# Kernel tuning notes

Measured on AMD Instinct MI355X. Metric: run time of the kernel, lower is better.

The kernel has to match this reference:

```python
import jax, jax.numpy as jnp
import numpy as np

N_NODES = 100000
N_EDGES = 2000000
D_IN = 4
HID = 64


def setup_inputs() -> dict:
    key = jax.random.key(0)
    ks = jax.random.split(key, 8)
    node_feats = jax.random.normal(ks[0], (N_NODES, D_IN), dtype=jnp.float32)
    pairs = jax.random.randint(ks[1], (N_EDGES, 2), 0, N_NODES, dtype=jnp.int64)
    # Kaiming-ish init scaling
    W1 = jax.random.normal(ks[2], (D_IN, HID), dtype=jnp.float32) / np.sqrt(D_IN)
    b1 = jnp.zeros((HID,), dtype=jnp.float32)
    W2 = jax.random.normal(ks[3], (HID, HID), dtype=jnp.float32) / np.sqrt(HID)
    b2 = jnp.zeros((HID,), dtype=jnp.float32)
    We1 = jax.random.normal(ks[4], (3 * HID, HID), dtype=jnp.float32) / np.sqrt(3 * HID)
    be1 = jnp.zeros((HID,), dtype=jnp.float32)
    We2 = jax.random.normal(ks[5], (HID, 1), dtype=jnp.float32) / np.sqrt(HID)
    be2 = jnp.zeros((1,), dtype=jnp.float32)
    return {"node_feats": node_feats, "pairs": pairs, "W1": W1, "b1": b1,
            "W2": W2, "b2": b2, "We1": We1, "be1": be1, "We2": We2, "be2": be2}


def reference(node_feats, pairs, W1, b1, W2, b2, We1, be1, We2, be2):
    # node MLP: Linear -> ReLU -> Linear -> ReLU
    H = jax.nn.relu(node_feats @ W1 + b1)      # [N, HID]
    H = jax.nn.relu(H @ W2 + b2)               # [N, HID]
    # vectorized gather over all edge pairs (replaces Python loop)
    hu = H[pairs[:, 0]]                        # [E, HID]
    hv = H[pairs[:, 1]]                        # [E, HID]
    E = jnp.concatenate([hu, hv, jnp.abs(hu - hv)], axis=-1)  # [E, 3*HID]
    # edge MLP: Linear -> ReLU -> Linear, squeeze last dim
    scores = (jax.nn.relu(E @ We1 + be1) @ We2 + be2)[:, 0]   # [E]
    return scores
```

## Files before the change

### kernel.cpp

```cpp
#include <hip/hip_runtime.h>

#define N_NODES 100000
#define N_EDGES 2000000

typedef __bf16 bf16x8 __attribute__((ext_vector_type(8)));
typedef float f32x4 __attribute__((ext_vector_type(4)));
typedef float f32x16 __attribute__((ext_vector_type(16)));

__device__ __forceinline__ unsigned f2bf_rne(float f) {
  unsigned u = __builtin_bit_cast(unsigned, f);
  u += 0x7FFFu + ((u >> 16) & 1u);
  return u >> 16;
}

__device__ __forceinline__ unsigned pack_rhu(float lo, float hi) {
  unsigned ulo = __builtin_bit_cast(unsigned, lo) + 0x8000u;
  unsigned uhi = __builtin_bit_cast(unsigned, hi) + 0x8000u;
  return __builtin_amdgcn_perm(uhi, ulo, 0x07060302u);
}

__device__ __forceinline__ unsigned absdiff_pack(unsigned a, unsigned b) {
  float alo = __builtin_bit_cast(float, a << 16);
  float ahi = __builtin_bit_cast(float, a & 0xFFFF0000u);
  float blo = __builtin_bit_cast(float, b << 16);
  float bhi = __builtin_bit_cast(float, b & 0xFFFF0000u);
  return pack_rhu(fabsf(alo - blo), fabsf(ahi - bhi));
}

__global__ __launch_bounds__(64, 1) void node_mfma_kernel(
    const float* __restrict__ X, const float* __restrict__ W1,
    const float* __restrict__ b1, const float* __restrict__ W2,
    const float* __restrict__ b2, unsigned short* __restrict__ H) {
  const int lane = threadIdx.x;
  const int l15 = lane & 15;
  const int quad = lane >> 4;

  float w1v[2][4][8], b1v[2][8];
#pragma unroll
  for (int c = 0; c < 2; ++c)
#pragma unroll
    for (int j = 0; j < 8; ++j) {
      int col = c * 32 + quad * 8 + j;
      b1v[c][j] = b1[col];
#pragma unroll
      for (int d = 0; d < 4; ++d) w1v[c][d][j] = W1[d * 64 + col];
    }

  uint4 afr[2][4];
#pragma unroll
  for (int c = 0; c < 2; ++c)
#pragma unroll
    for (int mt = 0; mt < 4; ++mt) {
      unsigned w[4];
#pragma unroll
      for (int p = 0; p < 4; ++p) {
        int k = c * 32 + quad * 8 + 2 * p;
        unsigned lo = f2bf_rne(W2[k * 64 + mt * 16 + l15]);
        unsigned hi = f2bf_rne(W2[(k + 1) * 64 + mt * 16 + l15]);
        w[p] = lo | (hi << 16);
      }
      afr[c][mt] = make_uint4(w[0], w[1], w[2], w[3]);
    }
  float b2v[16];
#pragma unroll
  for (int mt = 0; mt < 4; ++mt)
#pragma unroll
    for (int r = 0; r < 4; ++r) b2v[mt * 4 + r] = b2[mt * 16 + quad * 4 + r];

  const int ntiles = N_NODES / 16;
  for (int tile = blockIdx.x; tile < ntiles; tile += gridDim.x) {
    float4 xv = ((const float4*)X)[tile * 16 + l15];

    uint4 bfr[2];
#pragma unroll
    for (int c = 0; c < 2; ++c) {
      unsigned w[4];
#pragma unroll
      for (int p = 0; p < 4; ++p) {
        float h0 = fmaxf(b1v[c][2 * p] + xv.x * w1v[c][0][2 * p] +
                             xv.y * w1v[c][1][2 * p] + xv.z * w1v[c][2][2 * p] +
                             xv.w * w1v[c][3][2 * p],
                         0.f);
        float h1 = fmaxf(b1v[c][2 * p + 1] + xv.x * w1v[c][0][2 * p + 1] +
                             xv.y * w1v[c][1][2 * p + 1] +
                             xv.z * w1v[c][2][2 * p + 1] +
                             xv.w * w1v[c][3][2 * p + 1],
                         0.f);
        w[p] = pack_rhu(h0, h1);
      }
      bfr[c] = make_uint4(w[0], w[1], w[2], w[3]);
    }

    f32x4 acc[4];
#pragma unroll
    for (int mt = 0; mt < 4; ++mt) acc[mt] = (f32x4){0.f, 0.f, 0.f, 0.f};
#pragma unroll
    for (int c = 0; c < 2; ++c)
#pragma unroll
      for (int mt = 0; mt < 4; ++mt)
        acc[mt] = __builtin_amdgcn_mfma_f32_16x16x32_bf16(
            __builtin_bit_cast(bf16x8, afr[c][mt]),
            __builtin_bit_cast(bf16x8, bfr[c]), acc[mt], 0, 0, 0);

    unsigned short* hrow = H + (tile * 16 + l15) * 64;
#pragma unroll
    for (int mt = 0; mt < 4; ++mt) {
      unsigned lo = pack_rhu(fmaxf(acc[mt][0] + b2v[mt * 4 + 0], 0.f),
                             fmaxf(acc[mt][1] + b2v[mt * 4 + 1], 0.f));
      unsigned hi = pack_rhu(fmaxf(acc[mt][2] + b2v[mt * 4 + 2], 0.f),
                             fmaxf(acc[mt][3] + b2v[mt * 4 + 3], 0.f));
      *(uint2*)(hrow + mt * 16 + quad * 4) = make_uint2(lo, hi);
    }
  }
}

__global__ __launch_bounds__(256, 2) void edge_mlp_kernel(
    const unsigned short* __restrict__ H, const int* __restrict__ pairs,
    const float* __restrict__ We1, const float* __restrict__ be1,
    const float* __restrict__ We2, const float* __restrict__ be2,
    float* __restrict__ out) {
  __shared__ uint4 wlds[26 * 64];
  const int tid = threadIdx.x;

  for (int s = tid; s < 26 * 64; s += 256) {
    int f = s >> 6, ln = s & 63;
    int c = f >> 1, mt = f & 1;
    int col = mt * 32 + (ln & 31);
    uint4 val;
    if (c < 12) {
      int kb = c * 16 + (ln >> 5) * 8;
      val.x = f2bf_rne(We1[(kb + 0) * 64 + col]) |
              (f2bf_rne(We1[(kb + 1) * 64 + col]) << 16);
      val.y = f2bf_rne(We1[(kb + 2) * 64 + col]) |
              (f2bf_rne(We1[(kb + 3) * 64 + col]) << 16);
      val.z = f2bf_rne(We1[(kb + 4) * 64 + col]) |
              (f2bf_rne(We1[(kb + 5) * 64 + col]) << 16);
      val.w = f2bf_rne(We1[(kb + 6) * 64 + col]) |
              (f2bf_rne(We1[(kb + 7) * 64 + col]) << 16);
    } else {
      val.x = ((ln >> 5) == 0) ? f2bf_rne(be1[col]) : 0u;
      val.y = 0u;
      val.z = 0u;
      val.w = 0u;
    }
    wlds[s] = val;
  }

  const int lane = tid & 63;
  const int n = lane & 31;
  const int half = lane >> 5;

  uint4 b13u = make_uint4((half == 0) ? 0x00003F80u : 0u, 0u, 0u, 0u);

  float we2v[32];
#pragma unroll
  for (int mt = 0; mt < 2; ++mt)
#pragma unroll
    for (int r = 0; r < 16; ++r)
      we2v[mt * 16 + r] = We2[mt * 32 + (r & 3) + 8 * (r >> 2) + 4 * half];
  const float be2v = be2[0];
  __syncthreads();

  const int wid = blockIdx.x * 4 + (tid >> 6);
  const int nw = gridDim.x * 4;
  const int ntiles = N_EDGES / 32;
  const int last = ntiles - 1;
  const int2* pairs2 = (const int2*)pairs;
  const uint4* wf = wlds + lane;

  uint4 g[2][8];
  int2 uvn[2];
#pragma unroll
  for (int k = 0; k < 2; ++k) {
    int t = wid + k * nw;
    t = (t <= last) ? t : last;
    int2 uv = pairs2[t * 32 + n];
    const uint4* pu = (const uint4*)(H + uv.x * 64 + half * 8);
    const uint4* pv = (const uint4*)(H + uv.y * 64 + half * 8);
#pragma unroll
    for (int c = 0; c < 4; ++c) {
      g[k][c] = pu[c * 2];
      g[k][4 + c] = pv[c * 2];
    }
    int tn = wid + (k + 2) * nw;
    tn = (tn <= last) ? tn : last;
    uvn[k] = pairs2[tn * 32 + n];
  }

  for (int base = wid; base < ntiles; base += 2 * nw) {
#pragma unroll
    for (int k = 0; k < 2; ++k) {
      int t = base + k * nw;
      t = (t <= last) ? t : last;

      uint4 ab[4];
#pragma unroll
      for (int c = 0; c < 4; ++c) {
        ab[c].x = absdiff_pack(g[k][c].x, g[k][4 + c].x);
        ab[c].y = absdiff_pack(g[k][c].y, g[k][4 + c].y);
        ab[c].z = absdiff_pack(g[k][c].z, g[k][4 + c].z);
        ab[c].w = absdiff_pack(g[k][c].w, g[k][4 + c].w);
      }

      f32x16 acc[2];
      acc[0] = (f32x16)(0.f);
      acc[1] = (f32x16)(0.f);
#pragma unroll
      for (int c = 0; c < 13; ++c) {
        uint4 bu = (c < 8) ? g[k][c] : (c < 12 ? ab[c - 8] : b13u);
        bf16x8 b = __builtin_bit_cast(bf16x8, bu);
#pragma unroll
        for (int mt = 0; mt < 2; ++mt) {
          bf16x8 a = __builtin_bit_cast(bf16x8, wf[(c * 2 + mt) * 64]);
          acc[mt] = __builtin_amdgcn_mfma_f32_32x32x16_bf16(a, b, acc[mt], 0,
                                                            0, 0);
        }
      }

      {
        const uint4* qu = (const uint4*)(H + uvn[k].x * 64 + half * 8);
        const uint4* qv = (const uint4*)(H + uvn[k].y * 64 + half * 8);
#pragma unroll
        for (int c = 0; c < 4; ++c) {
          g[k][c] = qu[c * 2];
          g[k][4 + c] = qv[c * 2];
        }
        int tn = base + (k + 4) * nw;
        tn = (tn <= last) ? tn : last;
        uvn[k] = pairs2[tn * 32 + n];
      }

      float s = 0.f;
#pragma unroll
      for (int mt = 0; mt < 2; ++mt)
#pragma unroll
        for (int r = 0; r < 16; ++r)
          s += fmaxf(acc[mt][r], 0.f) * we2v[mt * 16 + r];
      s += __shfl_xor(s, 32);
      if (half == 0) out[t * 32 + n] = s + be2v;
    }
  }
}

extern "C" void kernel_launch(void* const* d_in, const int* in_sizes, int n_in,
                              void* d_out, int out_size, void* d_ws,
                              size_t ws_size, hipStream_t stream) {
  const float* X = (const float*)d_in[0];
  const int* pairs = (const int*)d_in[1];
  const float* W1 = (const float*)d_in[2];
  const float* b1 = (const float*)d_in[3];
  const float* W2 = (const float*)d_in[4];
  const float* b2 = (const float*)d_in[5];
  const float* We1 = (const float*)d_in[6];
  const float* be1 = (const float*)d_in[7];
  const float* We2 = (const float*)d_in[8];
  const float* be2 = (const float*)d_in[9];
  float* out = (float*)d_out;
  unsigned short* H = (unsigned short*)d_ws;

  node_mfma_kernel<<<1024, 64, 0, stream>>>(X, W1, b1, W2, b2, H);
  edge_mlp_kernel<<<1024, 256, 0, stream>>>(H, pairs, We1, be1, We2, be2, out);
}
```

Measured before the change: 170.9 us.

## Gather node rows into swizzled LDS via global_load_lds with single-tile prefetch

The edge kernel now gathers the H rows for each tile straight into a per-wave, XOR-swizzled LDS buffer using global_load_lds, instead of loading them into registers with a two-tile software pipeline. Each 128-byte row is fetched with one coalesced set of 16-byte lanes, and the next tile's gathers are issued after the MFMA loop, with manual waitcnt and sched_barrier fencing. The grid is halved to 512 blocks. The aim is to cut register pressure and make the gathers more coalesced, at the cost of a shallower prefetch depth, extra LDS traffic and reliance on hand-written waitcnt encodings being correct.

```diff
diff --git a/kernel.cpp b/kernel.cpp
--- a/kernel.cpp
+++ b/kernel.cpp
@@ -6,6 +6,9 @@
 typedef __bf16 bf16x8 __attribute__((ext_vector_type(8)));
 typedef float f32x4 __attribute__((ext_vector_type(4)));
 typedef float f32x16 __attribute__((ext_vector_type(16)));
+
+#define AS1 __attribute__((address_space(1)))
+#define AS3 __attribute__((address_space(3)))
 
 __device__ __forceinline__ unsigned f2bf_rne(float f) {
   unsigned u = __builtin_bit_cast(unsigned, f);
@@ -120,6 +123,7 @@
     const float* __restrict__ We2, const float* __restrict__ be2,
     float* __restrict__ out) {
   __shared__ uint4 wlds[26 * 64];
+  __shared__ uint4 gbuf[4 * 512];
   const int tid = threadIdx.x;
 
   for (int s = tid; s < 26 * 64; s += 256) {
@@ -149,6 +153,11 @@
   const int lane = tid & 63;
   const int n = lane & 31;
   const int half = lane >> 5;
+  const int wave = tid >> 6;
+  const int rowsel = lane >> 3;
+  const int swzc = (lane & 7) ^ rowsel;
+
+  uint4* gw = &gbuf[wave * 512];
 
   uint4 b13u = make_uint4((half == 0) ? 0x00003F80u : 0u, 0u, 0u, 0u);
 
@@ -161,84 +170,98 @@
   const float be2v = be2[0];
   __syncthreads();
 
-  const int wid = blockIdx.x * 4 + (tid >> 6);
+  const uint4* rb[4];
+#pragma unroll
+  for (int c = 0; c < 4; ++c) rb[c] = gw + n * 8 + (((2 * c + half) ^ (n & 7)));
+
+  const int wid = blockIdx.x * 4 + wave;
   const int nw = gridDim.x * 4;
   const int ntiles = N_EDGES / 32;
   const int last = ntiles - 1;
   const int2* pairs2 = (const int2*)pairs;
-  const uint4* wf = wlds + lane;
-
-  uint4 g[2][8];
-  int2 uvn[2];
-#pragma unroll
-  for (int k = 0; k < 2; ++k) {
-    int t = wid + k * nw;
-    t = (t <= last) ? t : last;
-    int2 uv = pairs2[t * 32 + n];
-    const uint4* pu = (const uint4*)(H + uv.x * 64 + half * 8);
-    const uint4* pv = (const uint4*)(H + uv.y * 64 + half * 8);
+
+  auto issue_gathers = [&](int2 pr0, int2 pr1, int2 pr2, int2 pr3) {
+    int2 prs[4] = {pr0, pr1, pr2, pr3};
+#pragma unroll
+    for (int k = 0; k < 4; ++k) {
+      const AS1 unsigned* gu =
+          (const AS1 unsigned*)(H + (size_t)prs[k].x * 64) + swzc * 4;
+      const AS1 unsigned* gv =
+          (const AS1 unsigned*)(H + (size_t)prs[k].y * 64) + swzc * 4;
+      __builtin_amdgcn_global_load_lds(gu, (AS3 unsigned*)(gw + k * 64), 16, 0,
+                                       0);
+      __builtin_amdgcn_global_load_lds(gv,
+                                       (AS3 unsigned*)(gw + 256 + k * 64), 16,
+                                       0, 0);
+    }
+  };
+
+  int2 pr[4];
+  {
+    int t0 = wid;
+#pragma unroll
+    for (int k = 0; k < 4; ++k) pr[k] = pairs2[t0 * 32 + k * 8 + rowsel];
+    issue_gathers(pr[0], pr[1], pr[2], pr[3]);
+    int t1 = wid + nw <= last ? wid + nw : last;
+#pragma unroll
+    for (int k = 0; k < 4; ++k) pr[k] = pairs2[t1 * 32 + k * 8 + rowsel];
+  }
+
+  for (int tile = wid; tile < ntiles; tile += nw) {
+    __builtin_amdgcn_s_waitcnt(0x0F70);
+    __builtin_amdgcn_sched_barrier(0);
+
+    uint4 hu[4], hv[4];
 #pragma unroll
     for (int c = 0; c < 4; ++c) {
-      g[k][c] = pu[c * 2];
-      g[k][4 + c] = pv[c * 2];
-    }
-    int tn = wid + (k + 2) * nw;
-    tn = (tn <= last) ? tn : last;
-    uvn[k] = pairs2[tn * 32 + n];
-  }
-
-  for (int base = wid; base < ntiles; base += 2 * nw) {
-#pragma unroll
-    for (int k = 0; k < 2; ++k) {
-      int t = base + k * nw;
-      t = (t <= last) ? t : last;
-
-      uint4 ab[4];
-#pragma unroll
-      for (int c = 0; c < 4; ++c) {
-        ab[c].x = absdiff_pack(g[k][c].x, g[k][4 + c].x);
-        ab[c].y = absdiff_pack(g[k][c].y, g[k][4 + c].y);
-        ab[c].z = absdiff_pack(g[k][c].z, g[k][4 + c].z);
-        ab[c].w = absdiff_pack(g[k][c].w, g[k][4 + c].w);
+      hu[c] = rb[c][0];
+      hv[c] = rb[c][256];
+    }
+
+    uint4 ab[4];
+#pragma unroll
+    for (int c = 0; c < 4; ++c) {
+      ab[c].x = absdiff_pack(hu[c].x, hv[c].x);
+      ab[c].y = absdiff_pack(hu[c].y, hv[c].y);
+      ab[c].z = absdiff_pack(hu[c].z, hv[c].z);
+      ab[c].w = absdiff_pack(hu[c].w, hv[c].w);
+    }
+
+    f32x16 acc[2];
+    acc[0] = (f32x16)(0.f);
+    acc[1] = (f32x16)(0.f);
+    const uint4* wf = wlds + lane;
+#pragma unroll
+    for (int c = 0; c < 13; ++c) {
+      uint4 bu = (c < 4) ? hu[c]
+                         : (c < 8) ? hv[c - 4] : (c < 12 ? ab[c - 8] : b13u);
+      bf16x8 b = __builtin_bit_cast(bf16x8, bu);
+#pragma unroll
+      for (int mt = 0; mt < 2; ++mt) {
+        bf16x8 a = __builtin_bit_cast(bf16x8, wf[(c * 2 + mt) * 64]);
+        acc[mt] =
+            __builtin_amdgcn_mfma_f32_32x32x16_bf16(a, b, acc[mt], 0, 0, 0);
       }
-
-      f32x16 acc[2];
-      acc[0] = (f32x16)(0.f);
-      acc[1] = (f32x16)(0.f);
-#pragma unroll
-      for (int c = 0; c < 13; ++c) {
-        uint4 bu = (c < 8) ? g[k][c] : (c < 12 ? ab[c - 8] : b13u);
-        bf16x8 b = __builtin_bit_cast(bf16x8, bu);
-#pragma unroll
-        for (int mt = 0; mt < 2; ++mt) {
-          bf16x8 a = __builtin_bit_cast(bf16x8, wf[(c * 2 + mt) * 64]);
-          acc[mt] = __builtin_amdgcn_mfma_f32_32x32x16_bf16(a, b, acc[mt], 0,
-                                                            0, 0);
-        }
-      }
-
-      {
-        const uint4* qu = (const uint4*)(H + uvn[k].x * 64 + half * 8);
-        const uint4* qv = (const uint4*)(H + uvn[k].y * 64 + half * 8);
-#pragma unroll
-        for (int c = 0; c < 4; ++c) {
-          g[k][c] = qu[c * 2];
-          g[k][4 + c] = qv[c * 2];
-        }
-        int tn = base + (k + 4) * nw;
-        tn = (tn <= last) ? tn : last;
-        uvn[k] = pairs2[tn * 32 + n];
-      }
-
-      float s = 0.f;
-#pragma unroll
-      for (int mt = 0; mt < 2; ++mt)
-#pragma unroll
-        for (int r = 0; r < 16; ++r)
-          s += fmaxf(acc[mt][r], 0.f) * we2v[mt * 16 + r];
-      s += __shfl_xor(s, 32);
-      if (half == 0) out[t * 32 + n] = s + be2v;
-    }
+    }
+
+    __builtin_amdgcn_s_waitcnt(0xC07F);
+    __builtin_amdgcn_sched_barrier(0);
+
+    issue_gathers(pr[0], pr[1], pr[2], pr[3]);
+    {
+      int t2 = tile + 2 * nw <= last ? tile + 2 * nw : last;
+#pragma unroll
+      for (int k = 0; k < 4; ++k) pr[k] = pairs2[t2 * 32 + k * 8 + rowsel];
+    }
+
+    float s = 0.f;
+#pragma unroll
+    for (int mt = 0; mt < 2; ++mt)
+#pragma unroll
+      for (int r = 0; r < 16; ++r)
+        s += fmaxf(acc[mt][r], 0.f) * we2v[mt * 16 + r];
+    s += __shfl_xor(s, 32);
+    if (half == 0) out[tile * 32 + n] = s + be2v;
   }
 }
 
@@ -259,5 +282,5 @@
   unsigned short* H = (unsigned short*)d_ws;
 
   node_mfma_kernel<<<1024, 64, 0, stream>>>(X, W1, b1, W2, b2, H);
-  edge_mlp_kernel<<<1024, 256, 0, stream>>>(H, pairs, We1, be1, We2, be2, out);
-}
+  edge_mlp_kernel<<<512, 256, 0, stream>>>(H, pairs, We1, be1, We2, be2, out);
+}
```

After: 164.4 us. -3.8%, faster.
